# Optimization experiments

Hardware: AMD Instinct MI355X
Metric: run time of the kernel (lower is better)

Reference implementation:

```python
import jax, jax.numpy as jnp
import numpy as np

STATE_DIM = 128
NUM_STATES = 16
BATCH = 16384


def setup_inputs() -> dict:
    key = jax.random.key(0)
    k1, k2, k3, k4 = jax.random.split(key, 4)
    x = jax.random.normal(k1, (BATCH, STATE_DIM), dtype=jnp.float32)
    state_idx = jax.random.randint(k2, (BATCH,), 0, NUM_STATES)
    A_all = jax.random.normal(k3, (NUM_STATES, STATE_DIM, STATE_DIM), dtype=jnp.float32)
    C_all = jax.random.normal(k4, (NUM_STATES, STATE_DIM, STATE_DIM), dtype=jnp.float32)
    return {"x": x, "state_idx": state_idx, "A_all": A_all, "C_all": C_all}


def reference(x, state_idx, A_all, C_all):
    # Per-sample expert matrix gather: [B, D, D]
    Ag = A_all[state_idx]
    Cg = C_all[state_idx]
    # state = relu(x @ A_i) per sample, batched via einsum
    state = jax.nn.relu(jnp.einsum('bd,bde->be', x, Ag))
    # observation = state @ C_i
    out = jnp.einsum('be,bef->bf', state, Cg)
    return out
```

## Files before the change

kernel.cpp:

```cpp
#include <hip/hip_runtime.h>

#define D 128
#define NS 16
#define BATCH 16384
#define TILE 64

typedef __attribute__((ext_vector_type(8))) short short8;
typedef __attribute__((ext_vector_type(4))) float f32x4;

__device__ __forceinline__ unsigned short f2bf(float f) {
  unsigned u = __builtin_bit_cast(unsigned, f);
  u += 0x7FFFu + ((u >> 16) & 1u);
  return (unsigned short)(u >> 16);
}

#define CPAD 32

__global__ __launch_bounds__(256) void prep_kernel(
    const float* __restrict__ A_all, const float* __restrict__ C_all,
    const int* __restrict__ sidx,
    int* __restrict__ counts, unsigned short* __restrict__ lists,
    unsigned short* __restrict__ At, unsigned short* __restrict__ Ct) {
  const int b = blockIdx.x, tid = threadIdx.x;
  if (b < 128) {
    __shared__ float T[32][129];
    const int mat = b >> 6, r = b & 63, s = r >> 2, slab = r & 3;
    const float* in = (mat ? C_all : A_all) + (size_t)s * D * D;
    unsigned short* outp = (mat ? Ct : At) + (size_t)s * D * D;
    const int e0 = slab * 32;
    const int ecol = (tid & 7) * 4;
    const int drow = tid >> 3;
#pragma unroll
    for (int i = 0; i < 4; i++) {
      const int d = drow + 32 * i;
      const float4 v = *(const float4*)(in + (size_t)d * D + e0 + ecol);
      T[ecol + 0][d] = v.x;
      T[ecol + 1][d] = v.y;
      T[ecol + 2][d] = v.z;
      T[ecol + 3][d] = v.w;
    }
    __syncthreads();
    const int e = tid >> 3;
    const int d0 = (tid & 7) * 16;
    unsigned short p[16];
#pragma unroll
    for (int k = 0; k < 16; k++) p[k] = f2bf(T[e][d0 + k]);
    unsigned short* dst = outp + (size_t)(e0 + e) * D + d0;
    *(uint4*)(dst) = *(const uint4*)(p);
    *(uint4*)(dst + 8) = *(const uint4*)(p + 8);
  } else {
    __shared__ int wcnt[4][NS];
    __shared__ int woff[4][NS];
    __shared__ int sbase[NS];
    const int i = (b - 128) * 256 + tid;
    const int s = sidx[i];
    const int lane = tid & 63, w = tid >> 6;
    int myrank = 0;
#pragma unroll 1
    for (int ss = 0; ss < NS; ss++) {
      unsigned long long m = __ballot(s == ss);
      if (s == ss) myrank = (int)__popcll(m & ((1ull << lane) - 1ull));
      if (lane == 0) wcnt[w][ss] = (int)__popcll(m);
    }
    __syncthreads();
    if (tid < NS) {
      const int c0 = wcnt[0][tid], c1 = wcnt[1][tid];
      const int c2 = wcnt[2][tid], c3 = wcnt[3][tid];
      sbase[tid] = atomicAdd(&counts[tid * CPAD], c0 + c1 + c2 + c3);
      woff[0][tid] = 0;
      woff[1][tid] = c0;
      woff[2][tid] = c0 + c1;
      woff[3][tid] = c0 + c1 + c2;
    }
    __syncthreads();
    lists[(size_t)s * BATCH + sbase[s] + woff[w][s] + myrank] = (unsigned short)i;
  }
}

__global__ __launch_bounds__(256, 3) void ssm_kernel(
    const float* __restrict__ x,
    const int* __restrict__ counts,
    const unsigned short* __restrict__ lists,
    const unsigned short* __restrict__ At,
    const unsigned short* __restrict__ Ct,
    float* __restrict__ out) {
  __shared__ unsigned short Xs[TILE][136];
  __shared__ unsigned short Ws[D][136];
  __shared__ int rows[TILE];

  const int s = blockIdx.y;
  const int n = counts[s * CPAD];
  const int row0 = blockIdx.x * TILE;
  if (row0 >= n) return;
  const int nr = min(TILE, n - row0);
  const int tid = threadIdx.x;

  const size_t lb = (size_t)s * BATCH + row0;
  if (tid < TILE) rows[tid] = (tid < nr) ? (int)lists[lb + tid] : -1;

  {
    const int r = tid >> 2, q = tid & 3;
    const int rowid = (r < nr) ? (int)lists[lb + r] : -1;
    unsigned short* xr = &Xs[r][q * 32];
    if (rowid >= 0) {
      const float4* src = (const float4*)(x + (size_t)rowid * D + q * 32);
#pragma unroll
      for (int i = 0; i < 8; i++) {
        float4 v = src[i];
        ushort4 p;
        p.x = f2bf(v.x); p.y = f2bf(v.y); p.z = f2bf(v.z); p.w = f2bf(v.w);
        *(ushort4*)(xr + i * 4) = p;
      }
    } else {
      ushort4 z; z.x = z.y = z.z = z.w = 0;
#pragma unroll
      for (int i = 0; i < 8; i++) *(ushort4*)(xr + i * 4) = z;
    }
  }
  {
    const uint4* g = (const uint4*)(At + (size_t)s * D * D);
#pragma unroll
    for (int c = tid; c < 2048; c += 256)
      *(uint4*)&Ws[c >> 4][(c & 15) * 8] = g[c];
  }
  __syncthreads();

  const int lane = tid & 63, w = tid >> 6;
  const int l15 = lane & 15, quad = lane >> 4;

  f32x4 acc[8];
#pragma unroll
  for (int nb = 0; nb < 8; nb++) acc[nb] = (f32x4){0.f, 0.f, 0.f, 0.f};

#pragma unroll
  for (int kb = 0; kb < 4; kb++) {
    short8 aF = *(const short8*)&Xs[w * 16 + l15][kb * 32 + quad * 8];
#pragma unroll
    for (int nb = 0; nb < 8; nb++) {
      short8 bF = *(const short8*)&Ws[nb * 16 + l15][kb * 32 + quad * 8];
      acc[nb] = __builtin_amdgcn_mfma_f32_16x16x32_bf16(aF, bF, acc[nb], 0, 0, 0);
    }
  }
  __syncthreads();

#pragma unroll
  for (int nb = 0; nb < 8; nb++)
#pragma unroll
    for (int r = 0; r < 4; r++) {
      float v = acc[nb][r];
      Xs[w * 16 + quad * 4 + r][nb * 16 + l15] = f2bf(v > 0.f ? v : 0.f);
    }
  {
    const uint4* g = (const uint4*)(Ct + (size_t)s * D * D);
#pragma unroll
    for (int c = tid; c < 2048; c += 256)
      *(uint4*)&Ws[c >> 4][(c & 15) * 8] = g[c];
  }
  __syncthreads();

#pragma unroll
  for (int nb = 0; nb < 8; nb++) acc[nb] = (f32x4){0.f, 0.f, 0.f, 0.f};
#pragma unroll
  for (int kb = 0; kb < 4; kb++) {
    short8 aF = *(const short8*)&Xs[w * 16 + l15][kb * 32 + quad * 8];
#pragma unroll
    for (int nb = 0; nb < 8; nb++) {
      short8 bF = *(const short8*)&Ws[nb * 16 + l15][kb * 32 + quad * 8];
      acc[nb] = __builtin_amdgcn_mfma_f32_16x16x32_bf16(aF, bF, acc[nb], 0, 0, 0);
    }
  }

#pragma unroll
  for (int r = 0; r < 4; r++) {
    const int rl = w * 16 + quad * 4 + r;
    if (rl < nr) {
      float* orow = out + (size_t)rows[rl] * D + l15;
#pragma unroll
      for (int nb = 0; nb < 8; nb++) orow[nb * 16] = acc[nb][r];
    }
  }
}

extern "C" void kernel_launch(void* const* d_in, const int* in_sizes, int n_in,
                              void* d_out, int out_size, void* d_ws, size_t ws_size,
                              hipStream_t stream) {
  const float* x = (const float*)d_in[0];
  const int* sidx = (const int*)d_in[1];
  const float* A_all = (const float*)d_in[2];
  const float* C_all = (const float*)d_in[3];
  float* out = (float*)d_out;

  int* counts = (int*)d_ws;
  unsigned short* lists = (unsigned short*)((char*)d_ws + 2048);
  unsigned short* At = (unsigned short*)((char*)d_ws + 2048 + 512 * 1024);
  unsigned short* Ct = At + NS * D * D;

  hipMemsetAsync(counts, 0, 2048, stream);
  prep_kernel<<<192, 256, 0, stream>>>(A_all, C_all, sidx, counts, lists, At, Ct);
  ssm_kernel<<<dim3(BATCH / TILE, NS), 256, 0, stream>>>(x, counts, lists, At, Ct, out);
}
```

Baseline: 80.51 us.

## Use persistent grid-stride blocks with smaller tiles and register-prefetched C weights

The grid becomes 32 persistent blocks per state that stride over 32-row tiles, replacing the large mostly-empty grid of 64-row tiles that exit early. Work is split 2x2 across warps, and a separate hidden buffer Hs is added. Each block prefetches the C matrix into registers before the first GEMM so the load overlaps with compute. A and C are still reloaded into LDS on every tile, so weight traffic per row roughly doubles. The extra Hs buffer and the ctr registers also increase LDS and register pressure.

```diff
diff --git a/kernel.cpp b/kernel.cpp
--- a/kernel.cpp
+++ b/kernel.cpp
@@ -3,7 +3,8 @@
 #define D 128
 #define NS 16
 #define BATCH 16384
-#define TILE 64
+#define TILE 32
+#define NTB 32
 
 typedef __attribute__((ext_vector_type(8))) short short8;
 typedef __attribute__((ext_vector_type(4))) float f32x4;
@@ -85,98 +86,108 @@
     const unsigned short* __restrict__ Ct,
     float* __restrict__ out) {
   __shared__ unsigned short Xs[TILE][136];
+  __shared__ unsigned short Hs[TILE][136];
   __shared__ unsigned short Ws[D][136];
   __shared__ int rows[TILE];
 
   const int s = blockIdx.y;
   const int n = counts[s * CPAD];
-  const int row0 = blockIdx.x * TILE;
-  if (row0 >= n) return;
-  const int nr = min(TILE, n - row0);
   const int tid = threadIdx.x;
-
-  const size_t lb = (size_t)s * BATCH + row0;
-  if (tid < TILE) rows[tid] = (tid < nr) ? (int)lists[lb + tid] : -1;
-
-  {
-    const int r = tid >> 2, q = tid & 3;
-    const int rowid = (r < nr) ? (int)lists[lb + r] : -1;
-    unsigned short* xr = &Xs[r][q * 32];
-    if (rowid >= 0) {
-      const float4* src = (const float4*)(x + (size_t)rowid * D + q * 32);
-#pragma unroll
-      for (int i = 0; i < 8; i++) {
-        float4 v = src[i];
-        ushort4 p;
-        p.x = f2bf(v.x); p.y = f2bf(v.y); p.z = f2bf(v.z); p.w = f2bf(v.w);
-        *(ushort4*)(xr + i * 4) = p;
-      }
-    } else {
-      ushort4 z; z.x = z.y = z.z = z.w = 0;
-#pragma unroll
-      for (int i = 0; i < 8; i++) *(ushort4*)(xr + i * 4) = z;
-    }
-  }
-  {
-    const uint4* g = (const uint4*)(At + (size_t)s * D * D);
-#pragma unroll
-    for (int c = tid; c < 2048; c += 256)
-      *(uint4*)&Ws[c >> 4][(c & 15) * 8] = g[c];
-  }
-  __syncthreads();
-
   const int lane = tid & 63, w = tid >> 6;
   const int l15 = lane & 15, quad = lane >> 4;
-
-  f32x4 acc[8];
-#pragma unroll
-  for (int nb = 0; nb < 8; nb++) acc[nb] = (f32x4){0.f, 0.f, 0.f, 0.f};
-
-#pragma unroll
-  for (int kb = 0; kb < 4; kb++) {
-    short8 aF = *(const short8*)&Xs[w * 16 + l15][kb * 32 + quad * 8];
-#pragma unroll
-    for (int nb = 0; nb < 8; nb++) {
-      short8 bF = *(const short8*)&Ws[nb * 16 + l15][kb * 32 + quad * 8];
-      acc[nb] = __builtin_amdgcn_mfma_f32_16x16x32_bf16(aF, bF, acc[nb], 0, 0, 0);
-    }
-  }
-  __syncthreads();
-
-#pragma unroll
-  for (int nb = 0; nb < 8; nb++)
+  const int wr = w & 1, wc = w >> 1;
+
+  for (int t0 = blockIdx.x; t0 * TILE < n; t0 += NTB) {
+    if (t0 != blockIdx.x) __syncthreads();
+    const int row0 = t0 * TILE;
+    const int nr = min(TILE, n - row0);
+    const size_t lb = (size_t)s * BATCH + row0;
+
+    uint4 ctr[8];
+    {
+      const uint4* g = (const uint4*)(Ct + (size_t)s * D * D);
+#pragma unroll
+      for (int i = 0; i < 8; i++) ctr[i] = g[i * 256 + tid];
+    }
+
+    {
+      const int r = tid >> 3, q = tid & 7;
+      int rid = (r < nr) ? (int)lists[lb + r] : -1;
+      if (q == 0) rows[r] = rid;
+      unsigned short* xr = &Xs[r][q * 16];
+      if (rid >= 0) {
+        const float4* src = (const float4*)(x + (size_t)rid * D + q * 16);
+#pragma unroll
+        for (int i = 0; i < 4; i++) {
+          float4 v = src[i];
+          ushort4 p;
+          p.x = f2bf(v.x); p.y = f2bf(v.y); p.z = f2bf(v.z); p.w = f2bf(v.w);
+          *(ushort4*)(xr + i * 4) = p;
+        }
+      } else {
+        ushort4 z; z.x = z.y = z.z = z.w = 0;
+#pragma unroll
+        for (int i = 0; i < 4; i++) *(ushort4*)(xr + i * 4) = z;
+      }
+    }
+    {
+      const uint4* g = (const uint4*)(At + (size_t)s * D * D);
+#pragma unroll
+      for (int i = 0; i < 8; i++) {
+        const int c = i * 256 + tid;
+        *(uint4*)&Ws[c >> 4][(c & 15) * 8] = g[c];
+      }
+    }
+    __syncthreads();
+
+    f32x4 acc[4];
+#pragma unroll
+    for (int nb = 0; nb < 4; nb++) acc[nb] = (f32x4){0.f, 0.f, 0.f, 0.f};
+#pragma unroll
+    for (int kb = 0; kb < 4; kb++) {
+      short8 aF = *(const short8*)&Xs[wr * 16 + l15][kb * 32 + quad * 8];
+#pragma unroll
+      for (int nb = 0; nb < 4; nb++) {
+        short8 bF = *(const short8*)&Ws[wc * 64 + nb * 16 + l15][kb * 32 + quad * 8];
+        acc[nb] = __builtin_amdgcn_mfma_f32_16x16x32_bf16(aF, bF, acc[nb], 0, 0, 0);
+      }
+    }
+#pragma unroll
+    for (int nb = 0; nb < 4; nb++)
+#pragma unroll
+      for (int r = 0; r < 4; r++) {
+        float v = acc[nb][r];
+        Hs[wr * 16 + quad * 4 + r][wc * 64 + nb * 16 + l15] = f2bf(v > 0.f ? v : 0.f);
+      }
+    __syncthreads();
+
+#pragma unroll
+    for (int i = 0; i < 8; i++) {
+      const int c = i * 256 + tid;
+      *(uint4*)&Ws[c >> 4][(c & 15) * 8] = ctr[i];
+    }
+    __syncthreads();
+
+#pragma unroll
+    for (int nb = 0; nb < 4; nb++) acc[nb] = (f32x4){0.f, 0.f, 0.f, 0.f};
+#pragma unroll
+    for (int kb = 0; kb < 4; kb++) {
+      short8 aF = *(const short8*)&Hs[wr * 16 + l15][kb * 32 + quad * 8];
+#pragma unroll
+      for (int nb = 0; nb < 4; nb++) {
+        short8 bF = *(const short8*)&Ws[wc * 64 + nb * 16 + l15][kb * 32 + quad * 8];
+        acc[nb] = __builtin_amdgcn_mfma_f32_16x16x32_bf16(aF, bF, acc[nb], 0, 0, 0);
+      }
+    }
+
 #pragma unroll
     for (int r = 0; r < 4; r++) {
-      float v = acc[nb][r];
-      Xs[w * 16 + quad * 4 + r][nb * 16 + l15] = f2bf(v > 0.f ? v : 0.f);
-    }
-  {
-    const uint4* g = (const uint4*)(Ct + (size_t)s * D * D);
-#pragma unroll
-    for (int c = tid; c < 2048; c += 256)
-      *(uint4*)&Ws[c >> 4][(c & 15) * 8] = g[c];
-  }
-  __syncthreads();
-
-#pragma unroll
-  for (int nb = 0; nb < 8; nb++) acc[nb] = (f32x4){0.f, 0.f, 0.f, 0.f};
-#pragma unroll
-  for (int kb = 0; kb < 4; kb++) {
-    short8 aF = *(const short8*)&Xs[w * 16 + l15][kb * 32 + quad * 8];
-#pragma unroll
-    for (int nb = 0; nb < 8; nb++) {
-      short8 bF = *(const short8*)&Ws[nb * 16 + l15][kb * 32 + quad * 8];
-      acc[nb] = __builtin_amdgcn_mfma_f32_16x16x32_bf16(aF, bF, acc[nb], 0, 0, 0);
-    }
-  }
-
-#pragma unroll
-  for (int r = 0; r < 4; r++) {
-    const int rl = w * 16 + quad * 4 + r;
-    if (rl < nr) {
-      float* orow = out + (size_t)rows[rl] * D + l15;
-#pragma unroll
-      for (int nb = 0; nb < 8; nb++) orow[nb * 16] = acc[nb][r];
+      const int rl = wr * 16 + quad * 4 + r;
+      if (rl < nr) {
+        float* orow = out + (size_t)rows[rl] * D + wc * 64 + l15;
+#pragma unroll
+        for (int nb = 0; nb < 4; nb++) orow[nb * 16] = acc[nb][r];
+      }
     }
   }
 }
@@ -197,5 +208,5 @@
 
   hipMemsetAsync(counts, 0, 2048, stream);
   prep_kernel<<<192, 256, 0, stream>>>(A_all, C_all, sidx, counts, lists, At, Ct);
-  ssm_kernel<<<dim3(BATCH / TILE, NS), 256, 0, stream>>>(x, counts, lists, At, Ct, out);
-}
+  ssm_kernel<<<dim3(NTB, NS), 256, 0, stream>>>(x, counts, lists, At, Ct, out);
+}
```

Result: slower. 84.22 us (+4.6%).
